# Kernel tuning notes

Hardware: AMD Instinct MI355X
Metric: run time of the kernel (lower is better)

## Reference

```python
import jax, jax.numpy as jnp
import numpy as np

B, T, R, A = 4, 40, 2000, 36864
H = W = 64
C = 256
PP = 7
RED = 16.0
NCLS = 21
NPOS = 64   # rois_per_image*B//4
NNEG = 192  # rois_per_image*B*3//4
DH = 1024

def _iou(b1, b2):
    # boxes are (top,left,bottom,right)
    t = jnp.maximum(b1[..., 0], b2[..., 0])
    l = jnp.maximum(b1[..., 1], b2[..., 1])
    b = jnp.minimum(b1[..., 2], b2[..., 2])
    r = jnp.minimum(b1[..., 3], b2[..., 3])
    inter = jnp.clip(b - t, 0.0) * jnp.clip(r - l, 0.0)
    a1 = (b1[..., 2] - b1[..., 0]) * (b1[..., 3] - b1[..., 1])
    a2 = (b2[..., 2] - b2[..., 0]) * (b2[..., 3] - b2[..., 1])
    return inter / (a1 + a2 - inter)

def _smooth_l1(p, t):
    d = jnp.abs(p - t)
    return jnp.mean(jnp.where(d < 1.0, 0.5 * d * d, d - 0.5))

def _roi_pool(fm, rois):
    # fm [B,C,H,W], rois [N,5] = (img_id, top,left,bottom,right) in feature-map coords
    fmt = jnp.transpose(fm, (0, 2, 3, 1))  # [B,H,W,C]
    n = rois[:, 0].astype(jnp.int32)[:, None, None]
    t, l, b, r = rois[:, 1], rois[:, 2], rois[:, 3], rois[:, 4]
    g = (jnp.arange(PP, dtype=fm.dtype) + 0.5) / PP
    ys = jnp.clip(t[:, None] + g * (b - t)[:, None], 0.0, H - 1.0)
    xs = jnp.clip(l[:, None] + g * (r - l)[:, None], 0.0, W - 1.0)
    y0 = jnp.floor(ys).astype(jnp.int32)
    x0 = jnp.floor(xs).astype(jnp.int32)
    y1 = jnp.minimum(y0 + 1, H - 1)
    x1 = jnp.minimum(x0 + 1, W - 1)
    wy = (ys - y0)[:, :, None, None]
    wx = (xs - x0)[:, None, :, None]
    def gat(yi, xi):
        return fmt[n, yi[:, :, None], xi[:, None, :], :]  # [N,PP,PP,C]
    v = (gat(y0, x0) * (1 - wy) * (1 - wx) + gat(y0, x1) * (1 - wy) * wx
         + gat(y1, x0) * wy * (1 - wx) + gat(y1, x1) * wy * wx)
    return v.reshape(v.shape[0], -1)  # [N, PP*PP*C]

def _forward(nms_reg, nms_cls, feature_maps, bboxes, classes, anchors, rpn_reg, rpn_cls, W1, b1, Wr, br, Wc, bc):
    # ---------------- RPN trainer: anchor/target matching ----------------
    iou_a = _iou(bboxes[:, :, None, :], anchors[None, None, :, :])   # [B,T,A]
    max_iou = jnp.max(iou_a, axis=1)                                  # [B,A]
    tidx = jnp.argmax(iou_a, axis=1)
    max_tgt = jnp.take_along_axis(bboxes, jnp.broadcast_to(tidx[:, :, None], (B, A, 4)), axis=1)
    mask = (max_iou > 0.5).reshape(-1)
    pos = jnp.nonzero(mask, size=128)[0]        # first 128 positives, flat order (matches cls[mask][:128])
    neg = jnp.nonzero(~mask, size=256 - B)[0]   # torch quirk: 256 - len(mask_matched) = 256 - B
    clsf = rpn_cls.reshape(-1)
    logits = jnp.concatenate([clsf[pos], clsf[neg]])
    lbl = jnp.concatenate([jnp.ones(128, dtype=logits.dtype), jnp.zeros(256 - B, dtype=logits.dtype)])
    rpn_cls_loss = jnp.mean(jnp.maximum(logits, 0) - logits * lbl + jnp.log1p(jnp.exp(-jnp.abs(logits))))
    anc_f = jnp.broadcast_to(anchors[None], (B, A, 4)).reshape(-1, 4)
    rpn_reg_loss = _smooth_l1(rpn_reg.reshape(-1, 4)[pos], max_tgt.reshape(-1, 4)[pos] - anc_f[pos]) / 4.0

    # ------------- RCNN trainer: proposal matching + sampling -------------
    iou_r = _iou(nms_reg[:, None, :, :], bboxes[:, :, None, :])  # [B,T,R]
    iou_m = jnp.max(iou_r, axis=1)                               # [B,R]
    ridx = jnp.argmax(iou_r, axis=1)
    iou_f = iou_m.reshape(-1)
    posr = jnp.nonzero(iou_f > 0.5, size=NPOS)[0]                # first NPOS positives, flat order
    negscore = jnp.where(iou_f <= 0.5, iou_f, -jnp.inf)
    negr = jax.lax.top_k(negscore, NNEG)[1]                      # negatives sorted by IoU descending
    cls_g = jnp.take_along_axis(classes, ridx, axis=1).reshape(-1)
    cls_s = jnp.concatenate([cls_g[posr], jnp.zeros(NNEG, dtype=cls_g.dtype)])
    imid = jnp.repeat(jnp.arange(B, dtype=nms_reg.dtype), R)
    nmsf = nms_reg.reshape(-1, 4)
    sel = jnp.concatenate([posr, negr])
    rois = jnp.concatenate([imid[sel][:, None], nmsf[sel]], axis=1)  # [256,5]
    feat = _roi_pool(feature_maps, rois)
    hmid = jax.nn.relu(feat @ W1 + b1)
    rreg = hmid @ Wr + br
    rcls = hmid @ Wc + bc
    logp = jax.nn.log_softmax(rcls, axis=-1)
    rcnn_cls_loss = -jnp.mean(jnp.take_along_axis(logp, cls_s[:, None], axis=1))
    posb = nmsf[posr]
    rounded = jnp.concatenate([jnp.floor(posb[:, :2] * RED), jnp.ceil(posb[:, 2:] * RED)], axis=1) / RED
    mb = jnp.take_along_axis(bboxes, jnp.broadcast_to(ridx[:, :, None], (B, R, 4)), axis=1).reshape(-1, 4)[posr]
    tgt = mb - rounded
    pr = rreg[:NPOS]
    rcnn_reg_loss = sum(_smooth_l1(pr[:, c], tgt[:, c]) for c in range(4)) / 4.0
    offset = sum(jnp.mean(jnp.abs(pr[:, c] - tgt[:, c])) for c in range(4)) / 4.0
    acc = jnp.mean((jnp.argmax(rcls[:NPOS], axis=-1) == cls_s[:NPOS]).astype(jnp.float32))
    return rpn_cls_loss, rpn_reg_loss, rcnn_cls_loss, rcnn_reg_loss, acc, offset

def _boxes(k, shape):
    k1, k2 = jax.random.split(k)
    c = jax.random.uniform(k1, shape + (2,), minval=10.0, maxval=54.0)
    h = jax.random.uniform(k2, shape + (2,), minval=3.0, maxval=8.0)
    return jnp.concatenate([c - h, c + h], axis=-1)  # (top,left,bottom,right)

def setup_inputs():
    key = jax.random.key(0)
    ks = jax.random.split(key, 13)
    base = _boxes(ks[0], (T,))
    shift = jax.random.uniform(ks[1], (B, T, 2), minval=-0.2, maxval=0.2)
    bboxes = base[None] + jnp.concatenate([shift, shift], axis=-1)  # guarantees >=128 RPN positives
    classes = jax.random.randint(ks[2], (B, T), 1, NCLS)
    anchors = _boxes(ks[3], (A,)).at[:T].set(base)
    nms_reg = _boxes(ks[4], (B, R))
    shift2 = jax.random.uniform(ks[5], (B, T, 2), minval=-0.1, maxval=0.1)
    nms_reg = nms_reg.at[:, :T].set(bboxes + jnp.concatenate([shift2, shift2], axis=-1))  # >=64 RCNN positives
    nms_cls = jax.random.normal(ks[6], (B, R))
    feature_maps = jax.random.normal(ks[7], (B, C, H, W))
    rpn_reg = 0.1 * jax.random.normal(ks[8], (B, A, 4))
    rpn_cls = jax.random.normal(ks[9], (B, A))
    D = PP * PP * C
    W1 = jax.random.normal(ks[10], (D, DH)) * float(1.0 / np.sqrt(D))
    b1 = jnp.zeros((DH,))
    Wr = jax.random.normal(ks[11], (DH, 4)) * float(1.0 / np.sqrt(DH))
    br = jnp.zeros((4,))
    Wc = jax.random.normal(ks[12], (DH, NCLS)) * float(1.0 / np.sqrt(DH))
    bc = jnp.zeros((NCLS,))
    return dict(nms_reg=nms_reg, nms_cls=nms_cls, feature_maps=feature_maps, bboxes=bboxes,
                classes=classes, anchors=anchors, rpn_reg=rpn_reg, rpn_cls=rpn_cls,
                W1=W1, b1=b1, Wr=Wr, br=br, Wc=Wc, bc=bc)

def reference(nms_reg, nms_cls, feature_maps, bboxes, classes, anchors, rpn_reg, rpn_cls, W1, b1, Wr, br, Wc, bc):
    return _forward(nms_reg, nms_cls, feature_maps, bboxes, classes, anchors, rpn_reg, rpn_cls, W1, b1, Wr, br, Wc, bc)
```

## Files before the change

kernel.cpp:

```cpp
#include <hip/hip_runtime.h>

typedef unsigned short u16;
typedef unsigned long long u64;

constexpr int cB = 4, cT = 40, cR = 2000, cA = 36864;
constexpr int cH = 64, cW = 64, cC = 256, cPP = 7;
constexpr int cNCLS = 21, cNPOS = 64, cNNEG = 192, cDH = 1024;
constexpr int cD = cPP * cPP * cC;
constexpr int cBA = cB * cA;
constexpr int cBR = cB * cR;
constexpr int NW64 = cBA / 64;
constexpr int SPLITS = 14;
constexpr int KCH = cD / SPLITS;
constexpr int BK = 64;
constexpr int NITER = KCH / BK;
constexpr unsigned POSKEY = 0x007FFFFFu;

constexpr size_t O_TIDX  = 0;
constexpr size_t O_MASKW = 589824;
constexpr size_t O_KEYS  = 608256;
constexpr size_t O_RIDXG = 640256;
constexpr size_t O_SEL   = 672256;
constexpr size_t O_CLS   = 673280;
constexpr size_t O_ROIS  = 674304;
constexpr size_t O_TGT   = 678400;
constexpr size_t O_FMT   = 1048576;
constexpr size_t O_FEAT  = O_FMT + 8388608;
constexpr size_t O_CPART = O_FEAT + 6422528;

__device__ __forceinline__ float b2f(u16 u) {
  return __uint_as_float(((unsigned)u) << 16);
}
__device__ __forceinline__ u16 f2b(float f) {
  unsigned x = __float_as_uint(f);
  unsigned r = x + 0x7FFFu + ((x >> 16) & 1u);
  return (u16)(r >> 16);
}
__device__ __forceinline__ unsigned f2key(float f) {
  unsigned b = __float_as_uint(f);
  return b ^ ((b & 0x80000000u) ? 0xFFFFFFFFu : 0x80000000u);
}

typedef __attribute__((ext_vector_type(8))) short short8;
typedef __attribute__((ext_vector_type(4))) float f32x4;

__global__ __launch_bounds__(256) void k_front(
    const float* __restrict__ bboxes, const float* __restrict__ anchors,
    const float* __restrict__ nms_reg, const float* __restrict__ fm,
    int* __restrict__ tidx, u64* __restrict__ maskw,
    unsigned* __restrict__ keys, int* __restrict__ ridxg,
    u16* __restrict__ fmt) {
  __shared__ float sfm[64 * 65];
  int bid = blockIdx.x;
  if (bid < 576) {
    float* sb = sfm;
    int b = bid / 144;
    if (threadIdx.x < cT * 4) sb[threadIdx.x] = bboxes[b * cT * 4 + threadIdx.x];
    __syncthreads();
    int i = bid * 256 + threadIdx.x;
    int a = i - b * cA;
    float4 av = ((const float4*)anchors)[a];
    float at = av.x, al = av.y, ab = av.z, ar = av.w;
    float area_a = (ab - at) * (ar - al);
    float best = -1.0f; int bi = 0;
    for (int t = 0; t < cT; ++t) {
      float bt = sb[t * 4], bl = sb[t * 4 + 1], bbv = sb[t * 4 + 2], brv = sb[t * 4 + 3];
      float ih = fmaxf(fminf(bbv, ab) - fmaxf(bt, at), 0.0f);
      float iw = fmaxf(fminf(brv, ar) - fmaxf(bl, al), 0.0f);
      float inter = ih * iw;
      float a1 = (bbv - bt) * (brv - bl);
      float iou = inter / (a1 + area_a - inter);
      if (iou > best) { best = iou; bi = t; }
    }
    tidx[i] = bi;
    u64 bal = __ballot(best > 0.5f);
    if ((threadIdx.x & 63) == 0) maskw[i >> 6] = bal;
  } else if (bid < 608) {
    float* sb = sfm;
    for (int j = threadIdx.x; j < cB * cT * 4; j += 256) sb[j] = bboxes[j];
    __syncthreads();
    int i = (bid - 576) * 256 + threadIdx.x;
    if (i >= cBR) return;
    int b = i / cR;
    float4 nv = ((const float4*)nms_reg)[i];
    float nt = nv.x, nl = nv.y, nb = nv.z, nr = nv.w;
    float area_n = (nb - nt) * (nr - nl);
    float best = -1.0f; int bi = 0;
    for (int t = 0; t < cT; ++t) {
      const float* bx = &sb[(b * cT + t) * 4];
      float ih = fmaxf(fminf(bx[2], nb) - fmaxf(bx[0], nt), 0.0f);
      float iw = fmaxf(fminf(bx[3], nr) - fmaxf(bx[1], nl), 0.0f);
      float inter = ih * iw;
      float a1 = (bx[2] - bx[0]) * (bx[3] - bx[1]);
      float iou = inter / (a1 + area_n - inter);
      if (iou > best) { best = iou; bi = t; }
    }
    keys[i] = (best <= 0.5f) ? f2key(best) : POSKEY;
    ridxg[i] = bi;
  } else {
    int f = bid - 608;
    int b = f >> 8;
    int c0 = ((f >> 6) & 3) * 64;
    int p0 = (f & 63) * 64;
    int t = threadIdx.x;
    int pL = (t & 15) * 4, cL = t >> 4;
    #pragma unroll
    for (int i = 0; i < 4; ++i) {
      int c = cL + i * 16;
      float4 v = *(const float4*)&fm[((size_t)b * cC + c0 + c) * (cH * cW) + p0 + pL];
      sfm[c * 65 + pL] = v.x; sfm[c * 65 + pL + 1] = v.y;
      sfm[c * 65 + pL + 2] = v.z; sfm[c * 65 + pL + 3] = v.w;
    }
    __syncthreads();
    int pW = t >> 2, cg = (t & 3) * 16;
    unsigned pk[8];
    #pragma unroll
    for (int j = 0; j < 8; ++j) {
      unsigned lo = f2b(sfm[(cg + 2 * j) * 65 + pW]);
      unsigned hi = f2b(sfm[(cg + 2 * j + 1) * 65 + pW]);
      pk[j] = lo | (hi << 16);
    }
    u16* dst = &fmt[((size_t)b * (cH * cW) + p0 + pW) * cC + c0 + cg];
    *(uint4*)dst = *(uint4*)&pk[0];
    *(uint4*)(dst + 8) = *(uint4*)&pk[4];
  }
}

__global__ __launch_bounds__(1024) void k_select(
    const u64* __restrict__ maskw, const int* __restrict__ tidx,
    const float* __restrict__ rpn_cls, const float* __restrict__ rpn_reg,
    const float* __restrict__ bboxes, const float* __restrict__ anchors,
    const unsigned* __restrict__ keysg, const int* __restrict__ ridxg,
    const float* __restrict__ nms_reg, const int* __restrict__ classes,
    int* __restrict__ sel, int* __restrict__ cls_s,
    float* __restrict__ rois, float* __restrict__ tgt,
    float* __restrict__ out) {
  __shared__ __align__(16) char smem[50688];
  __shared__ float s_scalF[2];
  __shared__ int s_scalI[3];
  int tid = threadIdx.x, lane = tid & 63, w = tid >> 6;
  u64 lmask = (1ULL << lane) - 1ULL;

  if (blockIdx.x == 0) {
    if (tid < 4) out[2 + tid] = 0.0f;
    u64* s_w   = (u64*)smem;
    int* s_pre = (int*)(smem + 18432);
    int* s_cw  = (int*)(smem + 19008);
    int* s_pos = (int*)(smem + 19584);
    int* s_neg = (int*)(smem + 20096);
    for (int k = tid; k < NW64; k += 1024) s_w[k] = maskw[k];
    if (tid < 128) s_pos[tid] = 0;
    if (tid < 252) s_neg[tid] = 0;
    if (tid == 0) { s_scalF[0] = 0.0f; s_scalF[1] = 0.0f; }
    __syncthreads();
    if (tid < 144) {
      int c = 0;
      #pragma unroll
      for (int k2 = 0; k2 < 16; ++k2) c += __popcll(s_w[tid * 16 + k2]);
      s_cw[tid] = c;
    }
    __syncthreads();
    if (tid == 0) {
      int run = 0;
      for (int ch = 0; ch < 144; ++ch) { s_pre[ch] = run; run += s_cw[ch]; }
    }
    __syncthreads();
    for (int ch = w; ch < 144; ch += 16) {
      int pbase = s_pre[ch];
      int nbase = ch * 1024 - pbase;
      if (pbase >= 128 && nbase >= 252) continue;
      int pc = 0;
      #pragma unroll
      for (int s2 = 0; s2 < 16; ++s2) {
        u64 word = s_w[ch * 16 + s2];
        bool m = (word >> lane) & 1ULL;
        int prefP = __popcll(word & lmask);
        int idx = ch * 1024 + s2 * 64 + lane;
        if (m) {
          int g = pbase + pc + prefP;
          if (g < 128) s_pos[g] = idx;
        } else {
          int g = nbase + (s2 * 64 + lane) - (pc + prefP);
          if (g < 252) s_neg[g] = idx;
        }
        pc += __popcll(word);
      }
    }
    __syncthreads();
    if (tid < 380) {
      int flat; float lbl;
      if (tid < 128) { flat = s_pos[tid]; lbl = 1.0f; }
      else           { flat = s_neg[tid - 128]; lbl = 0.0f; }
      float l = rpn_cls[flat];
      float term = fmaxf(l, 0.0f) - l * lbl + log1pf(expf(-fabsf(l)));
      atomicAdd(&s_scalF[0], term);
    }
    if (tid < 512) {
      int j = tid >> 2, c = tid & 3;
      int flat = s_pos[j];
      int b = flat / cA, a = flat - b * cA;
      int t = tidx[flat];
      float p = rpn_reg[flat * 4 + c];
      float tg = bboxes[(b * cT + t) * 4 + c] - anchors[a * 4 + c];
      float d = fabsf(p - tg);
      float sl = (d < 1.0f) ? 0.5f * d * d : d - 0.5f;
      atomicAdd(&s_scalF[1], sl);
    }
    __syncthreads();
    if (tid == 0) {
      out[0] = s_scalF[0] / 380.0f;
      out[1] = s_scalF[1] / 512.0f / 4.0f;
    }
  } else {
    unsigned* s_key = (unsigned*)smem;
    int* s_hist = (int*)(smem + 32000);
    int* s_pc   = (int*)(smem + 48384);
    int* s_wsum = (int*)(smem + 48896);
    int* s_wsuf = (int*)(smem + 48960);
    int* s_posr = (int*)(smem + 49024);
    int* s_negr = (int*)(smem + 49280);

    for (int i = tid; i < cBR; i += 1024) s_key[i] = keysg[i];
    if (tid < 64) s_posr[tid] = 0;
    __syncthreads();

    {
      int myv = 0; int mypre[8];
      #pragma unroll
      for (int p = 0; p < 8; ++p) {
        int i = p * 1024 + tid;
        bool v = (i < cBR) && (s_key[i] == POSKEY);
        u64 bal = __ballot(v);
        if (lane == 0) s_pc[p * 16 + w] = __popcll(bal);
        mypre[p] = __popcll(bal & lmask);
        myv |= v ? (1 << p) : 0;
      }
      __syncthreads();
      if (tid == 0) {
        int run = 0;
        for (int k = 0; k < 128; ++k) { int t = s_pc[k]; s_pc[k] = run; run += t; }
      }
      __syncthreads();
      #pragma unroll
      for (int p = 0; p < 8; ++p) {
        if (myv & (1 << p)) {
          int g = s_pc[p * 16 + w] + mypre[p];
          if (g < 64) s_posr[g] = p * 1024 + tid;
        }
      }
    }

    unsigned thr = 0; int G = 0;
    int need = cNNEG;
    #pragma unroll
    for (int lvl = 0; lvl < 3; ++lvl) {
      __syncthreads();
      #pragma unroll
      for (int k = 0; k < 4; ++k) s_hist[tid * 4 + k] = 0;
      __syncthreads();
      #pragma unroll
      for (int p = 0; p < 8; ++p) {
        int i = p * 1024 + tid;
        if (i < cBR) {
          unsigned key = s_key[i];
          int bkt = -1;
          if (lvl == 0) bkt = key >> 20;
          else if (lvl == 1) { if ((key >> 20) == (thr >> 20)) bkt = (key >> 8) & 0xFFF; }
          else { if ((key >> 8) == (thr >> 8)) bkt = (key & 0xFF) << 4; }
          if (bkt >= 0) atomicAdd(&s_hist[bkt], 1);
        }
      }
      __syncthreads();
      int local0 = s_hist[tid * 4 + 0], local1 = s_hist[tid * 4 + 1];
      int local2 = s_hist[tid * 4 + 2], local3 = s_hist[tid * 4 + 3];
      int lsum = local0 + local1 + local2 + local3;
      int x = lsum;
      #pragma unroll
      for (int off = 1; off < 64; off <<= 1) {
        int t = __shfl_down(x, off, 64);
        if (lane + off < 64) x += t;
      }
      if (lane == 0) s_wsum[w] = x;
      __syncthreads();
      if (tid == 0) {
        int run = 0;
        for (int wi = 15; wi >= 0; --wi) { s_wsuf[wi] = run; run += s_wsum[wi]; }
      }
      __syncthreads();
      int above = s_wsuf[w] + (x - lsum);
      int run = above;
      int loc[4] = {local3, local2, local1, local0};
      #pragma unroll
      for (int j = 0; j < 4; ++j) {
        int S = run + loc[j];
        if (run < need && S >= need) { s_scalI[0] = tid * 4 + (3 - j); s_scalI[1] = run; }
        run = S;
      }
      __syncthreads();
      int bS = s_scalI[0], ov = s_scalI[1];
      if (lvl == 0) thr = ((unsigned)bS) << 20;
      else if (lvl == 1) thr |= ((unsigned)bS) << 8;
      else thr |= ((unsigned)bS) >> 4;
      G += ov;
      need -= ov;
    }

    if (tid == 0) s_scalI[2] = 0;
    __syncthreads();
    #pragma unroll
    for (int p = 0; p < 8; ++p) {
      int i = p * 1024 + tid;
      if (i < cBR && s_key[i] > thr) {
        int slot = atomicAdd(&s_scalI[2], 1);
        s_negr[slot] = i;
      }
    }
    {
      __syncthreads();
      int myv = 0; int mypre[8];
      #pragma unroll
      for (int p = 0; p < 8; ++p) {
        int i = p * 1024 + tid;
        bool v = (i < cBR) && (s_key[i] == thr);
        u64 bal = __ballot(v);
        if (lane == 0) s_pc[p * 16 + w] = __popcll(bal);
        mypre[p] = __popcll(bal & lmask);
        myv |= v ? (1 << p) : 0;
      }
      __syncthreads();
      if (tid == 0) {
        int run = 0;
        for (int k = 0; k < 128; ++k) { int t = s_pc[k]; s_pc[k] = run; run += t; }
      }
      __syncthreads();
      #pragma unroll
      for (int p = 0; p < 8; ++p) {
        if (myv & (1 << p)) {
          int g = s_pc[p * 16 + w] + mypre[p];
          if (g < need) s_negr[G + g] = p * 1024 + tid;
        }
      }
    }
    __syncthreads();

    if (tid < 256) {
      int flat = (tid < 64) ? s_posr[tid] : s_negr[tid - 64];
      sel[tid] = flat;
      int b = flat / cR;
      #pragma unroll
      for (int c = 0; c < 4; ++c) rois[tid * 4 + c] = nms_reg[flat * 4 + c];
      cls_s[tid] = (tid < 64) ? classes[b * cT + ridxg[flat]] : 0;
      if (tid < 64) {
        int mt = ridxg[flat];
        #pragma unroll
        for (int c = 0; c < 4; ++c) {
          float v = nms_reg[flat * 4 + c];
          float rr = ((c < 2) ? floorf(v * 16.0f) : ceilf(v * 16.0f)) / 16.0f;
          float mbv = bboxes[(b * cT + mt) * 4 + c];
          tgt[tid * 4 + c] = mbv - rr;
        }
      }
    }
  }
}

__global__ void k_roi_pool(const u16* __restrict__ fmt, const float* __restrict__ rois,
                           const int* __restrict__ sel, u16* __restrict__ feat) {
  int j = blockIdx.x;
  int py = blockIdx.y;
  int c = threadIdx.x;
  int flat = sel[j];
  int n = flat / cR;
  float t = rois[j * 4 + 0], l = rois[j * 4 + 1];
  float bb = rois[j * 4 + 2], r = rois[j * 4 + 3];
  const u16* base = fmt + (size_t)n * (cH * cW) * cC;
  float gy = (py + 0.5f) / (float)cPP;
  float ys = fminf(fmaxf(t + gy * (bb - t), 0.0f), 63.0f);
  int y0 = (int)floorf(ys);
  int y1 = min(y0 + 1, 63);
  float wy = ys - (float)y0;
  #pragma unroll
  for (int px = 0; px < cPP; ++px) {
    float gx = (px + 0.5f) / (float)cPP;
    float xs = fminf(fmaxf(l + gx * (r - l), 0.0f), 63.0f);
    int x0 = (int)floorf(xs);
    int x1 = min(x0 + 1, 63);
    float wx = xs - (float)x0;
    float f00 = b2f(base[(y0 * cW + x0) * cC + c]);
    float f01 = b2f(base[(y0 * cW + x1) * cC + c]);
    float f10 = b2f(base[(y1 * cW + x0) * cC + c]);
    float f11 = b2f(base[(y1 * cW + x1) * cC + c]);
    float v = f00 * (1.0f - wy) * (1.0f - wx) + f01 * (1.0f - wy) * wx +
              f10 * wy * (1.0f - wx) + f11 * wy * wx;
    feat[((size_t)j * 49 + py * cPP + px) * cC + c] = f2b(v);
  }
}

__global__ __launch_bounds__(256) void k_gemm1(const u16* __restrict__ feat, const float* __restrict__ W1,
                                               float* __restrict__ Cpart) {
  __shared__ u16 As[64][72];
  __shared__ u16 Bs[32][72];
  int tid = threadIdx.x;
  int n0 = blockIdx.x * 32;
  int kb0 = blockIdx.y * KCH;
  int m0 = blockIdx.z * 64;
  int lane = tid & 63, w = tid >> 6;
  int r = lane & 15, q = lane >> 4;
  f32x4 acc0 = {}, acc1 = {};

  int am = tid >> 2, aj = (tid & 3) * 16;
  int bn = tid & 31, bk = (tid >> 5) * 8;

  const u16* ap = &feat[(size_t)(m0 + am) * cD + kb0 + aj];
  const float* bp = &W1[(size_t)(kb0 + bk) * cDH + n0 + bn];

  uint4 ra0 = *(const uint4*)ap;
  uint4 ra1 = *(const uint4*)(ap + 8);
  float f0 = bp[0], f1 = bp[cDH], f2 = bp[2 * cDH], f3 = bp[3 * cDH];
  float f4 = bp[4 * cDH], f5 = bp[5 * cDH], f6 = bp[6 * cDH], f7 = bp[7 * cDH];

  for (int it = 0; it < NITER; ++it) {
    __syncthreads();
    *(uint4*)&As[am][aj] = ra0;
    *(uint4*)&As[am][aj + 8] = ra1;
    {
      union { u16 u[8]; uint4 v; } pb;
      pb.u[0] = f2b(f0); pb.u[1] = f2b(f1); pb.u[2] = f2b(f2); pb.u[3] = f2b(f3);
      pb.u[4] = f2b(f4); pb.u[5] = f2b(f5); pb.u[6] = f2b(f6); pb.u[7] = f2b(f7);
      *(uint4*)&Bs[bn][bk] = pb.v;
    }
    __syncthreads();
    if (it + 1 < NITER) {
      ap += BK;
      bp += (size_t)BK * cDH;
      ra0 = *(const uint4*)ap;
      ra1 = *(const uint4*)(ap + 8);
      f0 = bp[0]; f1 = bp[cDH]; f2 = bp[2 * cDH]; f3 = bp[3 * cDH];
      f4 = bp[4 * cDH]; f5 = bp[5 * cDH]; f6 = bp[6 * cDH]; f7 = bp[7 * cDH];
    }
    #pragma unroll
    for (int ks = 0; ks < 2; ++ks) {
      short8 a = *(const short8*)&As[w * 16 + r][ks * 32 + q * 8];
      short8 b0v = *(const short8*)&Bs[r][ks * 32 + q * 8];
      short8 b1v = *(const short8*)&Bs[16 + r][ks * 32 + q * 8];
      acc0 = __builtin_amdgcn_mfma_f32_16x16x32_bf16(a, b0v, acc0, 0, 0, 0);
      acc1 = __builtin_amdgcn_mfma_f32_16x16x32_bf16(a, b1v, acc1, 0, 0, 0);
    }
  }

  float* Cp = Cpart + (size_t)blockIdx.y * 256 * cDH;
  #pragma unroll
  for (int rg = 0; rg < 4; ++rg) {
    int row = m0 + w * 16 + q * 4 + rg;
    Cp[(size_t)row * cDH + n0 + r] = acc0[rg];
    Cp[(size_t)row * cDH + n0 + 16 + r] = acc1[rg];
  }
}

__global__ __launch_bounds__(256) void k_heads(
    const float* __restrict__ Cpart, const float* __restrict__ b1,
    const float* __restrict__ Wr, const float* __restrict__ br,
    const float* __restrict__ Wc, const float* __restrict__ bc,
    const int* __restrict__ cls_s, const float* __restrict__ tgt,
    float* __restrict__ out) {
  __shared__ float sacc[25];
  int row = blockIdx.x, tid = threadIdx.x, lane = tid & 63;
  if (tid < 25) sacc[tid] = 0.0f;
  __syncthreads();
  int k0 = tid * 4;
  float4 h = *(const float4*)&b1[k0];
  #pragma unroll
  for (int s = 0; s < SPLITS; ++s) {
    float4 c = *(const float4*)&Cpart[(size_t)s * 256 * cDH + (size_t)row * cDH + k0];
    h.x += c.x; h.y += c.y; h.z += c.z; h.w += c.w;
  }
  float hv[4] = {fmaxf(h.x, 0.f), fmaxf(h.y, 0.f), fmaxf(h.z, 0.f), fmaxf(h.w, 0.f)};
  float part[25];
  #pragma unroll
  for (int c = 0; c < 25; ++c) part[c] = 0.0f;
  #pragma unroll
  for (int j = 0; j < 4; ++j) {
    float4 wr = *(const float4*)&Wr[(k0 + j) * 4];
    part[0] += hv[j] * wr.x; part[1] += hv[j] * wr.y;
    part[2] += hv[j] * wr.z; part[3] += hv[j] * wr.w;
    const float* wc = &Wc[(k0 + j) * 21];
    #pragma unroll
    for (int c = 0; c < 21; ++c) part[4 + c] += hv[j] * wc[c];
  }
  #pragma unroll
  for (int off = 32; off; off >>= 1) {
    #pragma unroll
    for (int c = 0; c < 25; ++c) part[c] += __shfl_down(part[c], off, 64);
  }
  if (lane == 0) {
    #pragma unroll
    for (int c = 0; c < 25; ++c) atomicAdd(&sacc[c], part[c]);
  }
  __syncthreads();
  if (tid == 0) {
    int cls = cls_s[row];
    float m = -INFINITY;
    float vals[21];
    #pragma unroll
    for (int c = 0; c < 21; ++c) { vals[c] = sacc[4 + c] + bc[c]; m = fmaxf(m, vals[c]); }
    float sum = 0.0f;
    #pragma unroll
    for (int c = 0; c < 21; ++c) sum += expf(vals[c] - m);
    float lse = m + logf(sum);
    atomicAdd(&out[2], (lse - vals[cls]) * (1.0f / 256.0f));
    if (row < 64) {
      int am2 = 0; float bv = vals[0];
      #pragma unroll
      for (int c = 1; c < 21; ++c) if (vals[c] > bv) { bv = vals[c]; am2 = c; }
      if (am2 == cls) atomicAdd(&out[4], 1.0f / 64.0f);
    }
  }
  if (tid == 1 && row < 64) {
    float sl = 0.0f, of = 0.0f;
    #pragma unroll
    for (int c = 0; c < 4; ++c) {
      float d = fabsf((sacc[c] + br[c]) - tgt[row * 4 + c]);
      sl += (d < 1.0f) ? 0.5f * d * d : d - 0.5f;
      of += d;
    }
    atomicAdd(&out[3], sl * (1.0f / 256.0f));
    atomicAdd(&out[5], of * (1.0f / 256.0f));
  }
}

extern "C" void kernel_launch(void* const* d_in, const int* in_sizes, int n_in,
                              void* d_out, int out_size, void* d_ws, size_t ws_size,
                              hipStream_t stream) {
  const float* nms_reg = (const float*)d_in[0];
  const float* fm      = (const float*)d_in[2];
  const float* bboxes  = (const float*)d_in[3];
  const int*   classes = (const int*)d_in[4];
  const float* anchors = (const float*)d_in[5];
  const float* rpn_reg = (const float*)d_in[6];
  const float* rpn_cls = (const float*)d_in[7];
  const float* W1      = (const float*)d_in[8];
  const float* b1      = (const float*)d_in[9];
  const float* Wr      = (const float*)d_in[10];
  const float* br      = (const float*)d_in[11];
  const float* Wc      = (const float*)d_in[12];
  const float* bc      = (const float*)d_in[13];
  float* out = (float*)d_out;
  char* ws = (char*)d_ws;

  int*      tidx  = (int*)(ws + O_TIDX);
  u64*      maskw = (u64*)(ws + O_MASKW);
  unsigned* keys  = (unsigned*)(ws + O_KEYS);
  int*      ridxg = (int*)(ws + O_RIDXG);
  int*      sel   = (int*)(ws + O_SEL);
  int*      clss  = (int*)(ws + O_CLS);
  float*    rois  = (float*)(ws + O_ROIS);
  float*    tgt   = (float*)(ws + O_TGT);
  u16*      fmt   = (u16*)(ws + O_FMT);
  u16*      feat  = (u16*)(ws + O_FEAT);
  float*    Cpart = (float*)(ws + O_CPART);

  k_front<<<608 + 1024, 256, 0, stream>>>(bboxes, anchors, nms_reg, fm,
                                          tidx, maskw, keys, ridxg, fmt);
  k_select<<<2, 1024, 0, stream>>>(maskw, tidx, rpn_cls, rpn_reg, bboxes, anchors,
                                   keys, ridxg, nms_reg, classes, sel, clss, rois, tgt, out);
  k_roi_pool<<<dim3(256, cPP), 256, 0, stream>>>(fmt, rois, sel, feat);
  k_gemm1<<<dim3(32, SPLITS, 4), 256, 0, stream>>>(feat, W1, Cpart);
  k_heads<<<256, 256, 0, stream>>>(Cpart, b1, Wr, br, Wc, bc, clss, tgt, out);
}
```

Measured before the change: 188.2 us.

## Double-buffer GEMM1 shared tiles with XOR-swizzled layout and deeper prefetch

Rewrites the k_gemm1 main loop to use two LDS buffers for the A and B tiles, processing two K-steps per iteration. Register prefetch now runs two tiles ahead, so global loads overlap MFMA work. The padded [72] rows become [64] rows with an XOR swizzle on 8-element chunks, avoiding LDS bank conflicts without padding. The cost is more registers and a loop that assumes NITER is even.

```diff
diff --git a/kernel.cpp b/kernel.cpp
--- a/kernel.cpp
+++ b/kernel.cpp
@@ -398,8 +398,8 @@
 
 __global__ __launch_bounds__(256) void k_gemm1(const u16* __restrict__ feat, const float* __restrict__ W1,
                                                float* __restrict__ Cpart) {
-  __shared__ u16 As[64][72];
-  __shared__ u16 Bs[32][72];
+  __shared__ u16 As[2][64][64];
+  __shared__ u16 Bs[2][32][64];
   int tid = threadIdx.x;
   int n0 = blockIdx.x * 32;
   int kb0 = blockIdx.y * KCH;
@@ -408,44 +408,105 @@
   int r = lane & 15, q = lane >> 4;
   f32x4 acc0 = {}, acc1 = {};
 
-  int am = tid >> 2, aj = (tid & 3) * 16;
-  int bn = tid & 31, bk = (tid >> 5) * 8;
-
-  const u16* ap = &feat[(size_t)(m0 + am) * cD + kb0 + aj];
-  const float* bp = &W1[(size_t)(kb0 + bk) * cDH + n0 + bn];
-
-  uint4 ra0 = *(const uint4*)ap;
-  uint4 ra1 = *(const uint4*)(ap + 8);
-  float f0 = bp[0], f1 = bp[cDH], f2 = bp[2 * cDH], f3 = bp[3 * cDH];
-  float f4 = bp[4 * cDH], f5 = bp[5 * cDH], f6 = bp[6 * cDH], f7 = bp[7 * cDH];
-
-  for (int it = 0; it < NITER; ++it) {
-    __syncthreads();
-    *(uint4*)&As[am][aj] = ra0;
-    *(uint4*)&As[am][aj + 8] = ra1;
+  int am = tid >> 2;
+  int ac0 = (tid & 3) * 2;
+  int asw = am & 7;
+  int ac0s = (ac0 ^ asw) * 8;
+  int ac1s = ((ac0 + 1) ^ asw) * 8;
+  int bn = tid & 31, bkc = tid >> 5;
+  int bcs = (bkc ^ (bn & 7)) * 8;
+
+  int rb = r & 7;
+  int arow = w * 16 + r;
+  int offK0 = ((0 * 4 + q) ^ rb) * 8;
+  int offK1 = ((1 * 4 + q) ^ rb) * 8;
+
+  const u16* ap = &feat[(size_t)(m0 + am) * cD + kb0 + ac0 * 8];
+  const float* bp = &W1[(size_t)(kb0 + bkc * 8) * cDH + n0 + bn];
+
+  uint4 ra0A, ra1A; float fA[8];
+  uint4 ra0B, ra1B; float fB[8];
+
+  ra0A = *(const uint4*)ap; ra1A = *(const uint4*)(ap + 8);
+  #pragma unroll
+  for (int j = 0; j < 8; ++j) fA[j] = bp[(size_t)j * cDH];
+  ap += BK; bp += (size_t)BK * cDH;
+  ra0B = *(const uint4*)ap; ra1B = *(const uint4*)(ap + 8);
+  #pragma unroll
+  for (int j = 0; j < 8; ++j) fB[j] = bp[(size_t)j * cDH];
+  ap += BK; bp += (size_t)BK * cDH;
+  *(uint4*)&As[0][am][ac0s] = ra0A;
+  *(uint4*)&As[0][am][ac1s] = ra1A;
+  {
+    union { u16 u[8]; uint4 v; } pb;
+    #pragma unroll
+    for (int j = 0; j < 8; ++j) pb.u[j] = f2b(fA[j]);
+    *(uint4*)&Bs[0][bn][bcs] = pb.v;
+  }
+  ra0A = *(const uint4*)ap; ra1A = *(const uint4*)(ap + 8);
+  #pragma unroll
+  for (int j = 0; j < 8; ++j) fA[j] = bp[(size_t)j * cDH];
+  ap += BK; bp += (size_t)BK * cDH;
+  __syncthreads();
+
+  #pragma unroll
+  for (int it = 0; it < NITER; it += 2) {
+    *(uint4*)&As[1][am][ac0s] = ra0B;
+    *(uint4*)&As[1][am][ac1s] = ra1B;
     {
       union { u16 u[8]; uint4 v; } pb;
-      pb.u[0] = f2b(f0); pb.u[1] = f2b(f1); pb.u[2] = f2b(f2); pb.u[3] = f2b(f3);
-      pb.u[4] = f2b(f4); pb.u[5] = f2b(f5); pb.u[6] = f2b(f6); pb.u[7] = f2b(f7);
-      *(uint4*)&Bs[bn][bk] = pb.v;
-    }
-    __syncthreads();
-    if (it + 1 < NITER) {
-      ap += BK;
-      bp += (size_t)BK * cDH;
-      ra0 = *(const uint4*)ap;
-      ra1 = *(const uint4*)(ap + 8);
-      f0 = bp[0]; f1 = bp[cDH]; f2 = bp[2 * cDH]; f3 = bp[3 * cDH];
-      f4 = bp[4 * cDH]; f5 = bp[5 * cDH]; f6 = bp[6 * cDH]; f7 = bp[7 * cDH];
-    }
-    #pragma unroll
-    for (int ks = 0; ks < 2; ++ks) {
-      short8 a = *(const short8*)&As[w * 16 + r][ks * 32 + q * 8];
-      short8 b0v = *(const short8*)&Bs[r][ks * 32 + q * 8];
-      short8 b1v = *(const short8*)&Bs[16 + r][ks * 32 + q * 8];
-      acc0 = __builtin_amdgcn_mfma_f32_16x16x32_bf16(a, b0v, acc0, 0, 0, 0);
-      acc1 = __builtin_amdgcn_mfma_f32_16x16x32_bf16(a, b1v, acc1, 0, 0, 0);
-    }
+      #pragma unroll
+      for (int j = 0; j < 8; ++j) pb.u[j] = f2b(fB[j]);
+      *(uint4*)&Bs[1][bn][bcs] = pb.v;
+    }
+    if (it + 3 < NITER) {
+      ra0B = *(const uint4*)ap; ra1B = *(const uint4*)(ap + 8);
+      #pragma unroll
+      for (int j = 0; j < 8; ++j) fB[j] = bp[(size_t)j * cDH];
+      ap += BK; bp += (size_t)BK * cDH;
+    }
+    {
+      short8 a0 = *(const short8*)&As[0][arow][offK0];
+      short8 b00 = *(const short8*)&Bs[0][r][offK0];
+      short8 b10 = *(const short8*)&Bs[0][16 + r][offK0];
+      acc0 = __builtin_amdgcn_mfma_f32_16x16x32_bf16(a0, b00, acc0, 0, 0, 0);
+      acc1 = __builtin_amdgcn_mfma_f32_16x16x32_bf16(a0, b10, acc1, 0, 0, 0);
+      short8 a1 = *(const short8*)&As[0][arow][offK1];
+      short8 b01 = *(const short8*)&Bs[0][r][offK1];
+      short8 b11 = *(const short8*)&Bs[0][16 + r][offK1];
+      acc0 = __builtin_amdgcn_mfma_f32_16x16x32_bf16(a1, b01, acc0, 0, 0, 0);
+      acc1 = __builtin_amdgcn_mfma_f32_16x16x32_bf16(a1, b11, acc1, 0, 0, 0);
+    }
+    __syncthreads();
+    if (it + 2 < NITER) {
+      *(uint4*)&As[0][am][ac0s] = ra0A;
+      *(uint4*)&As[0][am][ac1s] = ra1A;
+      {
+        union { u16 u[8]; uint4 v; } pb;
+        #pragma unroll
+        for (int j = 0; j < 8; ++j) pb.u[j] = f2b(fA[j]);
+        *(uint4*)&Bs[0][bn][bcs] = pb.v;
+      }
+      if (it + 4 < NITER) {
+        ra0A = *(const uint4*)ap; ra1A = *(const uint4*)(ap + 8);
+        #pragma unroll
+        for (int j = 0; j < 8; ++j) fA[j] = bp[(size_t)j * cDH];
+        ap += BK; bp += (size_t)BK * cDH;
+      }
+    }
+    {
+      short8 a0 = *(const short8*)&As[1][arow][offK0];
+      short8 b00 = *(const short8*)&Bs[1][r][offK0];
+      short8 b10 = *(const short8*)&Bs[1][16 + r][offK0];
+      acc0 = __builtin_amdgcn_mfma_f32_16x16x32_bf16(a0, b00, acc0, 0, 0, 0);
+      acc1 = __builtin_amdgcn_mfma_f32_16x16x32_bf16(a0, b10, acc1, 0, 0, 0);
+      short8 a1 = *(const short8*)&As[1][arow][offK1];
+      short8 b01 = *(const short8*)&Bs[1][r][offK1];
+      short8 b11 = *(const short8*)&Bs[1][16 + r][offK1];
+      acc0 = __builtin_amdgcn_mfma_f32_16x16x32_bf16(a1, b01, acc0, 0, 0, 0);
+      acc1 = __builtin_amdgcn_mfma_f32_16x16x32_bf16(a1, b11, acc1, 0, 0, 0);
+    }
+    __syncthreads();
   }
 
   float* Cp = Cpart + (size_t)blockIdx.y * 256 * cDH;
```

After: 193.1 us. 1.03x slower.

## Restructure GEMM1 to cover all 256 rows per block with double-buffered swizzled B tile

Applied to the files above, without the earlier changes.

Each GEMM1 block now computes all 256 M rows for its 32-column N slice and K split, instead of one 64-row slice. A fragments are loaded straight from global memory into registers, so the A staging through shared memory goes away. The B tile is converted to bf16 once per block, double-buffered in shared memory with an XOR swizzle, and software-pipelined across iterations. This removes the 4x redundant fp32 W1 reads and conversions and cuts barrier count. The cost is a smaller grid (448 blocks), more registers per thread from 8 accumulators plus prefetched A, and uncoalesced direct global A loads.

```diff
diff --git a/kernel.cpp b/kernel.cpp
--- a/kernel.cpp
+++ b/kernel.cpp
@@ -398,62 +398,95 @@
 
 __global__ __launch_bounds__(256) void k_gemm1(const u16* __restrict__ feat, const float* __restrict__ W1,
                                                float* __restrict__ Cpart) {
-  __shared__ u16 As[64][72];
-  __shared__ u16 Bs[32][72];
+  __shared__ u16 Bs[2][32][64];
   int tid = threadIdx.x;
-  int n0 = blockIdx.x * 32;
-  int kb0 = blockIdx.y * KCH;
-  int m0 = blockIdx.z * 64;
+  int bid = blockIdx.x;
+  int ksp = bid >> 5;
+  int n0 = (bid & 31) * 32;
+  int kb0 = ksp * KCH;
   int lane = tid & 63, w = tid >> 6;
   int r = lane & 15, q = lane >> 4;
-  f32x4 acc0 = {}, acc1 = {};
-
-  int am = tid >> 2, aj = (tid & 3) * 16;
-  int bn = tid & 31, bk = (tid >> 5) * 8;
-
-  const u16* ap = &feat[(size_t)(m0 + am) * cD + kb0 + aj];
-  const float* bp = &W1[(size_t)(kb0 + bk) * cDH + n0 + bn];
-
-  uint4 ra0 = *(const uint4*)ap;
-  uint4 ra1 = *(const uint4*)(ap + 8);
-  float f0 = bp[0], f1 = bp[cDH], f2 = bp[2 * cDH], f3 = bp[3 * cDH];
-  float f4 = bp[4 * cDH], f5 = bp[5 * cDH], f6 = bp[6 * cDH], f7 = bp[7 * cDH];
-
-  for (int it = 0; it < NITER; ++it) {
-    __syncthreads();
-    *(uint4*)&As[am][aj] = ra0;
-    *(uint4*)&As[am][aj + 8] = ra1;
-    {
-      union { u16 u[8]; uint4 v; } pb;
-      pb.u[0] = f2b(f0); pb.u[1] = f2b(f1); pb.u[2] = f2b(f2); pb.u[3] = f2b(f3);
-      pb.u[4] = f2b(f4); pb.u[5] = f2b(f5); pb.u[6] = f2b(f6); pb.u[7] = f2b(f7);
-      *(uint4*)&Bs[bn][bk] = pb.v;
-    }
-    __syncthreads();
-    if (it + 1 < NITER) {
-      ap += BK;
-      bp += (size_t)BK * cDH;
-      ra0 = *(const uint4*)ap;
-      ra1 = *(const uint4*)(ap + 8);
-      f0 = bp[0]; f1 = bp[cDH]; f2 = bp[2 * cDH]; f3 = bp[3 * cDH];
-      f4 = bp[4 * cDH]; f5 = bp[5 * cDH]; f6 = bp[6 * cDH]; f7 = bp[7 * cDH];
-    }
-    #pragma unroll
-    for (int ks = 0; ks < 2; ++ks) {
-      short8 a = *(const short8*)&As[w * 16 + r][ks * 32 + q * 8];
-      short8 b0v = *(const short8*)&Bs[r][ks * 32 + q * 8];
-      short8 b1v = *(const short8*)&Bs[16 + r][ks * 32 + q * 8];
-      acc0 = __builtin_amdgcn_mfma_f32_16x16x32_bf16(a, b0v, acc0, 0, 0, 0);
-      acc1 = __builtin_amdgcn_mfma_f32_16x16x32_bf16(a, b1v, acc1, 0, 0, 0);
-    }
-  }
-
-  float* Cp = Cpart + (size_t)blockIdx.y * 256 * cDH;
+  int rb = r & 7;
+
+  f32x4 acc[4][2] = {};
+
+  int bn = tid & 31, kq = tid >> 5;
+  int bswz = (kq ^ (bn & 7)) * 8;
+  const float* bp = &W1[(size_t)(kb0 + kq * 8) * cDH + n0 + bn];
+
+  int offK0 = (q ^ rb) * 8;
+  int offK1 = ((4 + q) ^ rb) * 8;
+
+  const u16* afp = &feat[(size_t)(w * 64 + r) * cD + kb0 + q * 8];
+
+  float fE[8], fO[8];
+  short8 aE[4][2], aO[4][2];
+
+#define LOADB(f) { \
+    _Pragma("unroll") \
+    for (int j = 0; j < 8; ++j) f[j] = bp[(size_t)j * cDH]; \
+    bp += (size_t)BK * cDH; }
+#define STOREB(buf, f) { \
+    union { u16 u[8]; uint4 v; } pb; \
+    _Pragma("unroll") \
+    for (int j = 0; j < 8; ++j) pb.u[j] = f2b(f[j]); \
+    *(uint4*)&Bs[buf][bn][bswz] = pb.v; }
+#define LOADA(dst, itv) { \
+    const u16* _p = afp + (itv) * 64; \
+    _Pragma("unroll") \
+    for (int mf = 0; mf < 4; ++mf) { \
+      dst[mf][0] = *(const short8*)(_p + (size_t)mf * 16 * cD); \
+      dst[mf][1] = *(const short8*)(_p + (size_t)mf * 16 * cD + 32); \
+    } }
+#define COMPUTE(buf, a) { \
+    short8 b00 = *(const short8*)&Bs[buf][r][offK0]; \
+    short8 b10 = *(const short8*)&Bs[buf][16 + r][offK0]; \
+    short8 b01 = *(const short8*)&Bs[buf][r][offK1]; \
+    short8 b11 = *(const short8*)&Bs[buf][16 + r][offK1]; \
+    _Pragma("unroll") \
+    for (int mf = 0; mf < 4; ++mf) { \
+      acc[mf][0] = __builtin_amdgcn_mfma_f32_16x16x32_bf16(a[mf][0], b00, acc[mf][0], 0, 0, 0); \
+      acc[mf][1] = __builtin_amdgcn_mfma_f32_16x16x32_bf16(a[mf][0], b10, acc[mf][1], 0, 0, 0); \
+      acc[mf][0] = __builtin_amdgcn_mfma_f32_16x16x32_bf16(a[mf][1], b01, acc[mf][0], 0, 0, 0); \
+      acc[mf][1] = __builtin_amdgcn_mfma_f32_16x16x32_bf16(a[mf][1], b11, acc[mf][1], 0, 0, 0); \
+    } }
+
+  LOADB(fE);
+  LOADB(fO);
+  STOREB(0, fE);
+  LOADA(aE, 0);
+  LOADB(fE);
+  __syncthreads();
+
+  for (int it = 0; it < NITER; it += 2) {
+    STOREB(1, fO);
+    if (it + 3 < NITER) LOADB(fO);
+    LOADA(aO, it + 1);
+    COMPUTE(0, aE);
+    __syncthreads();
+    if (it + 2 < NITER) {
+      STOREB(0, fE);
+      if (it + 4 < NITER) LOADB(fE);
+      LOADA(aE, it + 2);
+    }
+    COMPUTE(1, aO);
+    __syncthreads();
+  }
+
+#undef LOADB
+#undef STOREB
+#undef LOADA
+#undef COMPUTE
+
+  float* Cp = Cpart + (size_t)ksp * 256 * cDH;
   #pragma unroll
-  for (int rg = 0; rg < 4; ++rg) {
-    int row = m0 + w * 16 + q * 4 + rg;
-    Cp[(size_t)row * cDH + n0 + r] = acc0[rg];
-    Cp[(size_t)row * cDH + n0 + 16 + r] = acc1[rg];
+  for (int mf = 0; mf < 4; ++mf) {
+    #pragma unroll
+    for (int rg = 0; rg < 4; ++rg) {
+      int row = w * 64 + mf * 16 + q * 4 + rg;
+      Cp[(size_t)row * cDH + n0 + r] = acc[mf][0][rg];
+      Cp[(size_t)row * cDH + n0 + 16 + r] = acc[mf][1][rg];
+    }
   }
 }
 
@@ -564,6 +597,6 @@
   k_select<<<2, 1024, 0, stream>>>(maskw, tidx, rpn_cls, rpn_reg, bboxes, anchors,
                                    keys, ridxg, nms_reg, classes, sel, clss, rois, tgt, out);
   k_roi_pool<<<dim3(256, cPP), 256, 0, stream>>>(fmt, rois, sel, feat);
-  k_gemm1<<<dim3(32, SPLITS, 4), 256, 0, stream>>>(feat, W1, Cpart);
+  k_gemm1<<<448, 256, 0, stream>>>(feat, W1, Cpart);
   k_heads<<<256, 256, 0, stream>>>(Cpart, b1, Wr, br, Wc, bc, clss, tgt, out);
 }
```

After: 192.6 us. +2.4%, slower.
